# Optimization experiments

Hardware: AMD Instinct MI355X
Metric: run time of the kernel (lower is better)

Reference implementation:

```python
import jax, jax.numpy as jnp
import numpy as np

BSZ, NLVL, E, H, FFN = 8, 4, 512, 8, 2048
D = E // H
NNZ = 131072
LMAX = NNZ // BSZ  # equal per-batch counts -> static padded length
THETA = 10.0


def _layernorm(x, g, b):
    mu = x.mean(-1, keepdims=True)
    var = ((x - mu) ** 2).mean(-1, keepdims=True)
    return (x - mu) / jnp.sqrt(var + 1e-5) * g + b


def _rope(x, pos, freqs):
    # x: [N, E], pos: [N] float, freqs: [H, D/2] -> rotate interleaved pairs per head
    N = x.shape[0]
    nh, half = freqs.shape
    xr = x.reshape(N, nh, half, 2)
    ang = pos[:, None, None] * freqs[None]            # [N, H, D/2]
    c, s = jnp.cos(ang), jnp.sin(ang)
    x1, x2 = xr[..., 0], xr[..., 1]
    out = jnp.stack([x1 * c - x2 * s, x1 * s + x2 * c], axis=-1)
    return out.reshape(N, -1)


def setup_inputs() -> dict:
    key = jax.random.key(0)
    ks = jax.random.split(key, 8)
    bg = jax.random.normal(ks[0], (BSZ, NLVL, E), jnp.float32)
    feature_values = jax.random.normal(ks[1], (NNZ, E), jnp.float32)
    # coalesced sparse COO -> batch indices sorted; equal counts per batch for static shapes
    feature_batch_idx = (jnp.arange(NNZ, dtype=jnp.int32) // LMAX)
    feature_level_idx = jax.random.randint(ks[2], (NNZ,), 0, NLVL, dtype=jnp.int32)
    s = 1.0 / np.sqrt(E)
    Wq = jax.random.normal(ks[3], (E, E), jnp.float32) * s
    Wkv = jax.random.normal(ks[4], (E, 2 * E), jnp.float32) * s
    Wo = jax.random.normal(ks[5], (E, E), jnp.float32) * s
    freqs = THETA ** (-jnp.arange(D // 2, dtype=jnp.float32) * 2.0 / D)
    rope_freqs = jnp.tile(freqs[None, :], (H, 1))  # share_heads=False: per-head table
    ln_attn_g, ln_attn_b = jnp.ones(E, jnp.float32), jnp.zeros(E, jnp.float32)
    ln_ffn_g, ln_ffn_b = jnp.ones(E, jnp.float32), jnp.zeros(E, jnp.float32)
    W1 = jax.random.normal(ks[6], (E, FFN), jnp.float32) * s
    b1 = jnp.zeros(FFN, jnp.float32)
    W2 = jax.random.normal(ks[7], (FFN, E), jnp.float32) * (1.0 / np.sqrt(FFN))
    b2 = jnp.zeros(E, jnp.float32)
    return {
        'bg': bg, 'feature_values': feature_values,
        'feature_batch_idx': feature_batch_idx, 'feature_level_idx': feature_level_idx,
        'Wq': Wq, 'Wkv': Wkv, 'Wo': Wo, 'rope_freqs': rope_freqs,
        'ln_attn_g': ln_attn_g, 'ln_attn_b': ln_attn_b,
        'ln_ffn_g': ln_ffn_g, 'ln_ffn_b': ln_ffn_b,
        'W1': W1, 'b1': b1, 'W2': W2, 'b2': b2,
        'max_len': LMAX,
    }


def reference(bg, feature_values, feature_batch_idx, feature_level_idx,
              Wq, Wkv, Wo, rope_freqs, ln_attn_g, ln_attn_b,
              ln_ffn_g, ln_ffn_b, W1, b1, W2, b2, max_len):
    bsz, nlvl, e = bg.shape
    nh = rope_freqs.shape[0]
    d = e // nh
    nnz = feature_values.shape[0]

    # --- attention block (pre-norm) ---
    residual = bg
    x = _layernorm(bg, ln_attn_g, ln_attn_b)
    q = (x @ Wq).reshape(bsz * nlvl, e)
    kv = feature_values @ Wkv
    k, v = kv[:, :e], kv[:, e:]

    # RoPE on level indices (replicates original's repeat_interleave ordering: level = i // bsz)
    q_lvl = (jnp.arange(bsz * nlvl) // bsz).astype(jnp.float32)
    q = _rope(q, q_lvl, rope_freqs)
    k = _rope(k, feature_level_idx.astype(jnp.float32), rope_freqs)

    # concatenated (ragged) -> padded per batch
    counts = jax.ops.segment_sum(jnp.ones(nnz, jnp.int32), feature_batch_idx, num_segments=bsz)
    offsets = jnp.concatenate([jnp.zeros(1, jnp.int32), jnp.cumsum(counts)[:-1].astype(jnp.int32)])
    pos = jnp.arange(nnz, dtype=jnp.int32) - offsets[feature_batch_idx]
    k_pad = jnp.zeros((bsz, max_len, e), k.dtype).at[feature_batch_idx, pos].set(k)
    v_pad = jnp.zeros((bsz, max_len, e), v.dtype).at[feature_batch_idx, pos].set(v)
    pad_mask = jnp.arange(max_len)[None, :] >= counts[:, None]  # True at padding

    # SDPA
    qh = q.reshape(bsz, nlvl, nh, d).transpose(0, 2, 1, 3)
    kh = k_pad.reshape(bsz, max_len, nh, d).transpose(0, 2, 1, 3)
    vh = v_pad.reshape(bsz, max_len, nh, d).transpose(0, 2, 1, 3)
    scores = jnp.einsum('bhqd,bhkd->bhqk', qh, kh) / jnp.sqrt(jnp.asarray(d, qh.dtype))
    scores = jnp.where(pad_mask[:, None, None, :], -jnp.inf, scores)
    attn = jax.nn.softmax(scores, axis=-1)
    o = jnp.einsum('bhqk,bhkd->bhqd', attn, vh).transpose(0, 2, 1, 3).reshape(bsz, nlvl, e)
    o = o @ Wo + residual

    # --- FFN block (pre-norm) ---
    y = _layernorm(o, ln_ffn_g, ln_ffn_b)
    y = jax.nn.relu(y @ W1 + b1) @ W2 + b2
    return o + y
```

## Files before the change

### kernel.cpp

```cpp
#include <hip/hip_runtime.h>
#include <hip/hip_bf16.h>
#include <math.h>

#define BSZ 8
#define NLVL 4
#define E 512
#define H 8
#define D 64
#define FFN 2048
#define NNZ 131072
#define NQ 32
#define P32 32

typedef __attribute__((ext_vector_type(8))) short bf16x8;
typedef __attribute__((ext_vector_type(4))) float f32x4;

#define WS_QROT   16
#define WS_WSUM   (WS_QROT + NQ*E)
#define WS_OATT   (WS_WSUM + BSZ*P32*E)
#define WS_O2     (WS_OATT + NQ*E)
#define WS_Y      (WS_O2 + NQ*E)
#define WS_HID    (WS_Y + NQ*E)
#define WS_PART   (WS_HID + NQ*FFN)
#define WS_PLANE  (WS_PART + 32*BSZ*P32*E)
#define WS_WALL   (WS_PLANE + P32*NNZ)
#define WS_PBF    (WS_WALL + BSZ*128*512/2)

__device__ inline short f2bf(float x) {
    __hip_bfloat16 h = __float2bfloat16(x);
    union { __hip_bfloat16 v; short s; } u; u.v = h; return u.s;
}

__device__ inline bf16x8 cvt8(const float* p) {
    float4 x = *(const float4*)p;
    float4 y = *(const float4*)(p + 4);
    union { bf16x8 v; __hip_bfloat162 h[4]; } u;
    u.h[0] = __float22bfloat162_rn(float2{x.x, x.y});
    u.h[1] = __float22bfloat162_rn(float2{x.z, x.w});
    u.h[2] = __float22bfloat162_rn(float2{y.x, y.y});
    u.h[3] = __float22bfloat162_rn(float2{y.z, y.w});
    return u.v;
}

__global__ void k_zero(int* wsi) {
    if (blockIdx.x == 0 && threadIdx.x < 8) wsi[threadIdx.x] = 0;
}

__global__ void k_hist(const int* __restrict__ fb, int* wsi) {
    __shared__ int h[8];
    int t = threadIdx.x;
    if (t < 8) h[t] = 0;
    __syncthreads();
    for (int j = blockIdx.x * 256 + t; j < NNZ; j += gridDim.x * 256)
        atomicAdd(&h[fb[j]], 1);
    __syncthreads();
    if (t < 8) atomicAdd(&wsi[t], h[t]);
}

__global__ void k_off(int* wsi) {
    if (threadIdx.x == 0) {
        int run = 0;
        for (int b = 0; b < 8; b++) { wsi[8 + b] = run; run += wsi[b]; }
    }
}

__global__ void k_qrot(const float* __restrict__ bg, const float* __restrict__ Wq,
                       const float* __restrict__ rf, const float* __restrict__ g,
                       const float* __restrict__ bb, float* __restrict__ ws) {
    __shared__ float xr[E];
    __shared__ float qrow[E];
    __shared__ float red[8];
    int r = blockIdx.x, t = threadIdx.x;
    float v0 = bg[r * E + t], v1 = bg[r * E + t + 256];
    float s = v0 + v1;
    for (int o = 32; o > 0; o >>= 1) s += __shfl_down(s, o, 64);
    if ((t & 63) == 0) red[t >> 6] = s;
    __syncthreads();
    if (t == 0) red[0] = (red[0] + red[1] + red[2] + red[3]) * (1.0f / E);
    __syncthreads();
    float mu = red[0];
    __syncthreads();
    float d0 = v0 - mu, d1 = v1 - mu;
    s = d0 * d0 + d1 * d1;
    for (int o = 32; o > 0; o >>= 1) s += __shfl_down(s, o, 64);
    if ((t & 63) == 0) red[t >> 6] = s;
    __syncthreads();
    if (t == 0) red[0] = rsqrtf((red[0] + red[1] + red[2] + red[3]) * (1.0f / E) + 1e-5f);
    __syncthreads();
    float rstd = red[0];
    xr[t] = d0 * rstd * g[t] + bb[t];
    xr[t + 256] = d1 * rstd * g[t + 256] + bb[t + 256];
    __syncthreads();
    for (int half = 0; half < 2; half++) {
        int c = t + half * 256;
        float acc = 0.f;
        for (int e = 0; e < E; e++) acc += xr[e] * Wq[e * E + c];
        qrow[c] = acc;
    }
    __syncthreads();
    int c0 = 2 * t, c1 = c0 + 1;
    int h = c0 >> 6, ii = (c0 & 63) >> 1;
    float freq = rf[h * 32 + ii];
    float pos = (float)(r >> 3);
    float a = pos * freq, ca = cosf(a), sa = sinf(a);
    float x1 = qrow[c0], x2 = qrow[c1];
    float* qr = ws + WS_QROT + r * E;
    qr[c0] = x1 * ca - x2 * sa;
    qr[c1] = x1 * sa + x2 * ca;
}

__global__ void k_wtil(const float* __restrict__ Wkv, const float* __restrict__ rf,
                       const float* __restrict__ ws, short* __restrict__ wall) {
    __shared__ float u[D];
    int blk = blockIdx.x;
    int h = blk & 7, lvl = (blk >> 3) & 3, r = blk >> 5;
    int b = r >> 2, l = r & 3;
    int t = threadIdx.x;
    const float* qr = ws + WS_QROT + r * E + h * D;
    if (t < 32) {
        float freq = rf[h * 32 + t];
        float a = (float)lvl * freq;
        float ca = cosf(a), sa = sinf(a);
        float x1 = qr[2 * t], x2 = qr[2 * t + 1];
        u[2 * t] = x1 * ca + x2 * sa;
        u[2 * t + 1] = -x1 * sa + x2 * ca;
    }
    __syncthreads();
    int n = lvl * 32 + l * 8 + h;
    short* wrow_out = wall + ((size_t)(b * 128 + n)) * E;
    for (int rep = 0; rep < 8; rep++) {
        int e = t + rep * 64;
        const float* wrow = Wkv + (size_t)e * (2 * E) + h * D;
        float acc = 0.f;
#pragma unroll
        for (int c = 0; c < D; c++) acc += wrow[c] * u[c];
        wrow_out[e] = f2bf(acc * 0.125f);
    }
}

__global__ __launch_bounds__(256) void k_scores(
    const float* __restrict__ fv, const int* __restrict__ fb, const int* __restrict__ fl,
    const short* __restrict__ wall, float* __restrict__ pplane) {
    int t = threadIdx.x;
    int wave = t >> 6, lane = t & 63, col = lane & 15, quad = lane >> 4;
    int jbase = blockIdx.x * 128;
    int j0 = jbase + wave * 32;
    int b = fb[jbase];
    const short* wb = wall + (size_t)b * 128 * E + (size_t)col * E + quad * 8;
    const float* a0 = fv + (size_t)(j0 + col) * E + quad * 8;
    const float* a1 = a0 + (size_t)16 * E;
    f32x4 acc[2][8];
#pragma unroll
    for (int mt = 0; mt < 2; mt++)
#pragma unroll
        for (int nt = 0; nt < 8; nt++) acc[mt][nt] = f32x4{0.f, 0.f, 0.f, 0.f};
    for (int ks = 0; ks < 16; ks++) {
        int e0 = ks * 32;
        bf16x8 bfr[8];
#pragma unroll
        for (int nt = 0; nt < 8; nt++)
            bfr[nt] = *(const bf16x8*)(wb + (size_t)nt * 16 * E + e0);
        bf16x8 af0 = cvt8(a0 + e0);
        bf16x8 af1 = cvt8(a1 + e0);
#pragma unroll
        for (int nt = 0; nt < 8; nt++) {
            acc[0][nt] = __builtin_amdgcn_mfma_f32_16x16x32_bf16(af0, bfr[nt], acc[0][nt], 0, 0, 0);
            acc[1][nt] = __builtin_amdgcn_mfma_f32_16x16x32_bf16(af1, bfr[nt], acc[1][nt], 0, 0, 0);
        }
    }
#pragma unroll
    for (int mt = 0; mt < 2; mt++) {
        int kb = j0 + mt * 16 + quad * 4;
#pragma unroll
        for (int r = 0; r < 4; r++) {
            int key = kb + r;
            int lv = fl[key];
#pragma unroll
            for (int nt = 0; nt < 8; nt++) {
                if ((nt >> 1) == lv) {
                    int p = ((nt & 1) << 4) + col;
                    pplane[(size_t)p * NNZ + key] = acc[mt][nt][r];
                }
            }
        }
    }
}

__global__ void k_softmax(const int* __restrict__ wsi, const int* __restrict__ maxlen,
                          float* __restrict__ pplane, short* __restrict__ pbf) {
    __shared__ float red[8];
    int b = blockIdx.x >> 5, p = blockIdx.x & 31;
    int t = threadIdx.x;
    int cnt = wsi[b], ml = maxlen[0];
    int n = cnt < ml ? cnt : ml;
    int off = wsi[8 + b];
    float* base = pplane + (size_t)p * NNZ + off;
    short* basebf = pbf + (size_t)p * NNZ + off;
    float m = -1e30f;
    for (int j = t; j < n; j += 256) m = fmaxf(m, base[j]);
    for (int o = 32; o > 0; o >>= 1) m = fmaxf(m, __shfl_down(m, o, 64));
    if ((t & 63) == 0) red[t >> 6] = m;
    __syncthreads();
    if (t == 0) red[0] = fmaxf(fmaxf(red[0], red[1]), fmaxf(red[2], red[3]));
    __syncthreads();
    m = red[0];
    __syncthreads();
    float s = 0.f;
    for (int j = t; j < n; j += 256) s += expf(base[j] - m);
    for (int o = 32; o > 0; o >>= 1) s += __shfl_down(s, o, 64);
    if ((t & 63) == 0) red[t >> 6] = s;
    __syncthreads();
    if (t == 0) red[0] = red[0] + red[1] + red[2] + red[3];
    __syncthreads();
    float inv = 1.0f / red[0];
    for (int j = t; j < n; j += 256) {
        float w = expf(base[j] - m) * inv;
        base[j] = w;
        basebf[j] = f2bf(w);
    }
}

#define KP 40
__global__ __launch_bounds__(256) void k_pv(
    const float* __restrict__ fv, const short* __restrict__ pbf,
    const int* __restrict__ wsi, const int* __restrict__ maxlen,
    float* __restrict__ part) {
    __shared__ short Bt[256 * KP];
    int t = threadIdx.x;
    int b = blockIdx.x, kc = blockIdx.y, eh = blockIdx.z;
    int cnt = wsi[b], ml = maxlen[0];
    int lim = cnt < ml ? cnt : ml;
    int off = wsi[8 + b];
    int base = kc * 512;
    int wave = t >> 6, lane = t & 63, col = lane & 15, quad = lane >> 4;
    f32x4 acc[2][4];
#pragma unroll
    for (int mt = 0; mt < 2; mt++)
#pragma unroll
        for (int nt = 0; nt < 4; nt++) acc[mt][nt] = f32x4{0.f, 0.f, 0.f, 0.f};
    int nsteps = 0;
    if (base < lim) {
        int r = lim - base;
        nsteps = (r + 31) >> 5;
        if (nsteps > 16) nsteps = 16;
    }
    int sj = (t & 15) * 2;
    int se = (t >> 4) * 16;
    const short* ap0 = pbf + (size_t)col * NNZ + off + base + quad * 8;
    const short* ap1 = ap0 + (size_t)16 * NNZ;
    for (int ks = 0; ks < nsteps; ks++) {
        int kbeg = base + ks * 32;
        __syncthreads();
        {
            int j0g = off + kbeg + sj;
            int j1g = j0g + 1;
            if (j0g > NNZ - 1) j0g = NNZ - 1;
            if (j1g > NNZ - 1) j1g = NNZ - 1;
            const float* r0 = fv + (size_t)j0g * E + eh * 256 + se;
            const float* r1 = fv + (size_t)j1g * E + eh * 256 + se;
#pragma unroll
            for (int i = 0; i < 4; i++) {
                float4 x0 = *(const float4*)(r0 + i * 4);
                float4 x1 = *(const float4*)(r1 + i * 4);
                const float* f0 = (const float*)&x0;
                const float* f1 = (const float*)&x1;
#pragma unroll
                for (int q = 0; q < 4; q++) {
                    *(__hip_bfloat162*)&Bt[(se + i * 4 + q) * KP + sj] =
                        __float22bfloat162_rn(float2{f0[q], f1[q]});
                }
            }
        }
        __syncthreads();
        int rem = lim - kbeg;
        bf16x8 af0 = *(const bf16x8*)(ap0 + ks * 32);
        bf16x8 af1 = *(const bf16x8*)(ap1 + ks * 32);
        if (rem < 32) {
#pragma unroll
            for (int jj = 0; jj < 8; jj++)
                if (quad * 8 + jj >= rem) { af0[jj] = 0; af1[jj] = 0; }
        }
        const short* bb = &Bt[(wave * 64 + col) * KP + quad * 8];
#pragma unroll
        for (int nt = 0; nt < 4; nt++) {
            bf16x8 bfr = *(const bf16x8*)(bb + nt * 16 * KP);
            acc[0][nt] = __builtin_amdgcn_mfma_f32_16x16x32_bf16(af0, bfr, acc[0][nt], 0, 0, 0);
            acc[1][nt] = __builtin_amdgcn_mfma_f32_16x16x32_bf16(af1, bfr, acc[1][nt], 0, 0, 0);
        }
    }
    float* dst = part + ((size_t)(kc * BSZ + b) * P32) * E + eh * 256;
#pragma unroll
    for (int mt = 0; mt < 2; mt++)
#pragma unroll
        for (int nt = 0; nt < 4; nt++)
#pragma unroll
            for (int r = 0; r < 4; r++) {
                int p = mt * 16 + quad * 4 + r;
                int e = wave * 64 + nt * 16 + col;
                dst[(size_t)p * E + e] = acc[mt][nt][r];
            }
}

__global__ void k_pvred(const float* __restrict__ part, float* __restrict__ wsum) {
    int bp = blockIdx.x;
    int t = threadIdx.x;
    int b = bp >> 5, p = bp & 31;
    for (int half = 0; half < 2; half++) {
        int e = t + half * 256;
        float s = 0.f;
        for (int kc = 0; kc < 32; kc++)
            s += part[((size_t)(kc * BSZ + b) * P32 + p) * E + e];
        wsum[(size_t)bp * E + e] = s;
    }
}

__global__ void k_oproj(const float* __restrict__ wsum, const float* __restrict__ Wkv,
                        float* __restrict__ oatt) {
    __shared__ float Aw[NQ][E];
    int h = blockIdx.x >> 2, ct = blockIdx.x & 3;
    int t = threadIdx.x;
    {
        int rr = t >> 3, x = (t & 7) * 64;
        int row = (rr >> 2) * P32 + (rr & 3) * 8 + h;
#pragma unroll
        for (int q4 = 0; q4 < 16; q4++)
            *(float4*)&Aw[rr][x + q4 * 4] = *(const float4*)&wsum[(size_t)row * E + x + q4 * 4];
    }
    __syncthreads();
#pragma unroll
    for (int rep = 0; rep < 2; rep++) {
        int idx = rep * 256 + t;
        int rr = idx >> 4, cl = idx & 15;
        int c = h * D + ct * 16 + cl;
        float acc = 0.f;
        for (int e = 0; e < E; e++) acc += Aw[rr][e] * Wkv[(size_t)e * (2 * E) + E + c];
        oatt[rr * E + c] = acc;
    }
}

__global__ void k_wo(const float* __restrict__ oatt, const float* __restrict__ Wo,
                     const float* __restrict__ bg, float* __restrict__ o2) {
    __shared__ float Aw[NQ * E];
    int t = threadIdx.x;
#pragma unroll
    for (int q = 0; q < 16; q++) {
        int i = (q * 256 + t) * 4;
        *(float4*)&Aw[i] = *(const float4*)&oatt[i];
    }
    __syncthreads();
    int ct = blockIdx.x;
#pragma unroll
    for (int rep = 0; rep < 4; rep++) {
        int idx = rep * 256 + t;
        int rr = idx >> 5, cl = idx & 31;
        int c = ct * 32 + cl;
        float acc = bg[rr * E + c];
        for (int e = 0; e < E; e++) acc += Aw[rr * E + e] * Wo[(size_t)e * E + c];
        o2[rr * E + c] = acc;
    }
}

__global__ void k_ln2(const float* __restrict__ o2, const float* __restrict__ g,
                      const float* __restrict__ bb, float* __restrict__ y) {
    __shared__ float red[8];
    int r = blockIdx.x, t = threadIdx.x;
    float v0 = o2[r * E + t], v1 = o2[r * E + t + 256];
    float s = v0 + v1;
    for (int o = 32; o > 0; o >>= 1) s += __shfl_down(s, o, 64);
    if ((t & 63) == 0) red[t >> 6] = s;
    __syncthreads();
    if (t == 0) red[0] = (red[0] + red[1] + red[2] + red[3]) * (1.0f / E);
    __syncthreads();
    float mu = red[0];
    __syncthreads();
    float d0 = v0 - mu, d1 = v1 - mu;
    s = d0 * d0 + d1 * d1;
    for (int o = 32; o > 0; o >>= 1) s += __shfl_down(s, o, 64);
    if ((t & 63) == 0) red[t >> 6] = s;
    __syncthreads();
    if (t == 0) red[0] = rsqrtf((red[0] + red[1] + red[2] + red[3]) * (1.0f / E) + 1e-5f);
    __syncthreads();
    float rstd = red[0];
    y[r * E + t] = d0 * rstd * g[t] + bb[t];
    y[r * E + t + 256] = d1 * rstd * g[t + 256] + bb[t + 256];
}

__global__ void k_ffn1(const float* __restrict__ y, const float* __restrict__ W1,
                       const float* __restrict__ b1, float* __restrict__ hid) {
    __shared__ float Aw[NQ * E];
    int t = threadIdx.x;
#pragma unroll
    for (int q = 0; q < 16; q++) {
        int i = (q * 256 + t) * 4;
        *(float4*)&Aw[i] = *(const float4*)&y[i];
    }
    __syncthreads();
    int ft = blockIdx.x;
#pragma unroll
    for (int rep = 0; rep < 4; rep++) {
        int idx = rep * 256 + t;
        int rr = idx >> 5, fl = idx & 31;
        int f = ft * 32 + fl;
        float acc = b1[f];
        for (int e = 0; e < E; e++) acc += Aw[rr * E + e] * W1[(size_t)e * FFN + f];
        hid[rr * FFN + f] = fmaxf(acc, 0.f);
    }
}

__global__ void k_ffn2(const float* __restrict__ hid, const float* __restrict__ W2,
                       const float* __restrict__ b2, const float* __restrict__ o2,
                       float* __restrict__ out) {
    int ct = blockIdx.x;
    int t = threadIdx.x;
#pragma unroll
    for (int rep = 0; rep < 2; rep++) {
        int idx = rep * 256 + t;
        int rr = idx >> 4, cl = idx & 15;
        int c = ct * 16 + cl;
        float acc = b2[c] + o2[rr * E + c];
        for (int f = 0; f < FFN; f++) acc += hid[rr * FFN + f] * W2[(size_t)f * E + c];
        out[rr * E + c] = acc;
    }
}

extern "C" void kernel_launch(void* const* d_in, const int* in_sizes, int n_in,
                              void* d_out, int out_size, void* d_ws, size_t ws_size,
                              hipStream_t stream) {
    const float* bg  = (const float*)d_in[0];
    const float* fv  = (const float*)d_in[1];
    const int*   fb  = (const int*)d_in[2];
    const int*   fl  = (const int*)d_in[3];
    const float* Wq  = (const float*)d_in[4];
    const float* Wkv = (const float*)d_in[5];
    const float* Wo  = (const float*)d_in[6];
    const float* rf  = (const float*)d_in[7];
    const float* lag = (const float*)d_in[8];
    const float* lab = (const float*)d_in[9];
    const float* lfg = (const float*)d_in[10];
    const float* lfb = (const float*)d_in[11];
    const float* W1  = (const float*)d_in[12];
    const float* b1  = (const float*)d_in[13];
    const float* W2  = (const float*)d_in[14];
    const float* b2  = (const float*)d_in[15];
    const int* maxlen = (const int*)d_in[16];
    float* ws = (float*)d_ws;
    int* wsi = (int*)d_ws;
    short* wall = (short*)(ws + WS_WALL);
    short* pbf  = (short*)(ws + WS_PBF);
    float* out = (float*)d_out;

    hipLaunchKernelGGL(k_zero, dim3(1), dim3(64), 0, stream, wsi);
    hipLaunchKernelGGL(k_hist, dim3(128), dim3(256), 0, stream, fb, wsi);
    hipLaunchKernelGGL(k_off, dim3(1), dim3(64), 0, stream, wsi);
    hipLaunchKernelGGL(k_qrot, dim3(NQ), dim3(256), 0, stream, bg, Wq, rf, lag, lab, ws);
    hipLaunchKernelGGL(k_wtil, dim3(NQ * NLVL * H), dim3(64), 0, stream, Wkv, rf, ws, wall);
    hipLaunchKernelGGL(k_scores, dim3(NNZ / 128), dim3(256), 0, stream,
                       fv, fb, fl, wall, ws + WS_PLANE);
    hipLaunchKernelGGL(k_softmax, dim3(BSZ * P32), dim3(256), 0, stream,
                       wsi, maxlen, ws + WS_PLANE, pbf);
    hipLaunchKernelGGL(k_pv, dim3(BSZ, 32, 2), dim3(256), 0, stream,
                       fv, pbf, wsi, maxlen, ws + WS_PART);
    hipLaunchKernelGGL(k_pvred, dim3(BSZ * P32), dim3(256), 0, stream,
                       ws + WS_PART, ws + WS_WSUM);
    hipLaunchKernelGGL(k_oproj, dim3(H * 4), dim3(256), 0, stream,
                       ws + WS_WSUM, Wkv, ws + WS_OATT);
    hipLaunchKernelGGL(k_wo, dim3(16), dim3(256), 0, stream,
                       ws + WS_OATT, Wo, bg, ws + WS_O2);
    hipLaunchKernelGGL(k_ln2, dim3(NQ), dim3(256), 0, stream,
                       ws + WS_O2, lfg, lfb, ws + WS_Y);
    hipLaunchKernelGGL(k_ffn1, dim3(FFN / 32), dim3(256), 0, stream,
                       ws + WS_Y, W1, b1, ws + WS_HID);
    hipLaunchKernelGGL(k_ffn2, dim3(E / 16), dim3(256), 0, stream,
                       ws + WS_HID, W2, b2, ws + WS_O2, out);
}
```

Before: 879.0 us.

## Fuse scores, softmax and PV into a flash-style split-K attention kernel

Replaces the separate score GEMM, global softmax and PV kernels with one flash-attention kernel. Each block loads a 256-key chunk of feature values once, converts it to bf16 in shared memory in both row and transposed layouts, and computes scores and PV with an online softmax. Partial outputs and their max/sum statistics are then combined by a merge kernel. This avoids writing and re-reading the fp32 score plane and the bf16 probability plane, and reads the feature values once instead of twice. In exchange it adds more barriers per chunk, heavy shared-memory use, and a larger partial buffer to merge (64 chunks instead of 32).

```diff
diff --git a/kernel.cpp b/kernel.cpp
--- a/kernel.cpp
+++ b/kernel.cpp
@@ -11,6 +11,7 @@
 #define NNZ 131072
 #define NQ 32
 #define P32 32
+#define NEGF -3.0e38f
 
 typedef __attribute__((ext_vector_type(8))) short bf16x8;
 typedef __attribute__((ext_vector_type(4))) float f32x4;
@@ -22,24 +23,12 @@
 #define WS_Y      (WS_O2 + NQ*E)
 #define WS_HID    (WS_Y + NQ*E)
 #define WS_PART   (WS_HID + NQ*FFN)
-#define WS_PLANE  (WS_PART + 32*BSZ*P32*E)
-#define WS_WALL   (WS_PLANE + P32*NNZ)
-#define WS_PBF    (WS_WALL + BSZ*128*512/2)
+#define WS_ML     (WS_PART + 512*P32*E)
+#define WS_WALL   (WS_ML + 512*P32*2)
 
 __device__ inline short f2bf(float x) {
     __hip_bfloat16 h = __float2bfloat16(x);
     union { __hip_bfloat16 v; short s; } u; u.v = h; return u.s;
-}
-
-__device__ inline bf16x8 cvt8(const float* p) {
-    float4 x = *(const float4*)p;
-    float4 y = *(const float4*)(p + 4);
-    union { bf16x8 v; __hip_bfloat162 h[4]; } u;
-    u.h[0] = __float22bfloat162_rn(float2{x.x, x.y});
-    u.h[1] = __float22bfloat162_rn(float2{x.z, x.w});
-    u.h[2] = __float22bfloat162_rn(float2{y.x, y.y});
-    u.h[3] = __float22bfloat162_rn(float2{y.z, y.w});
-    return u.v;
 }
 
 __global__ void k_zero(int* wsi) {
@@ -138,179 +127,227 @@
     }
 }
 
-__global__ __launch_bounds__(256) void k_scores(
-    const float* __restrict__ fv, const int* __restrict__ fb, const int* __restrict__ fl,
-    const short* __restrict__ wall, float* __restrict__ pplane) {
-    int t = threadIdx.x;
-    int wave = t >> 6, lane = t & 63, col = lane & 15, quad = lane >> 4;
-    int jbase = blockIdx.x * 128;
-    int j0 = jbase + wave * 32;
-    int b = fb[jbase];
-    const short* wb = wall + (size_t)b * 128 * E + (size_t)col * E + quad * 8;
-    const float* a0 = fv + (size_t)(j0 + col) * E + quad * 8;
-    const float* a1 = a0 + (size_t)16 * E;
-    f32x4 acc[2][8];
+#define KSTR 520
+#define TSTR 40
+__global__ __launch_bounds__(256, 2) void k_flash(
+    const float* __restrict__ fv, const int* __restrict__ fl,
+    const short* __restrict__ wall, const int* __restrict__ wsi,
+    const int* __restrict__ maxlen, float* __restrict__ part, float* __restrict__ ml) {
+    __shared__ short kbuf[32 * KSTR];
+    __shared__ short fvT[512 * TSTR];
+    __shared__ short pbuf[32 * TSTR];
+    __shared__ float mbuf[4 * 32];
+    __shared__ float lpart[4 * 32];
+    __shared__ float alph[32];
+    __shared__ float mrun[32];
+    __shared__ float lrun[32];
+
+    int t = threadIdx.x;
+    int w = t >> 6, lane = t & 63, col = lane & 15, quad = lane >> 4;
+    int b = blockIdx.x, kc = blockIdx.y;
+    int cnt = wsi[b], mlen = maxlen[0];
+    int lim = cnt < mlen ? cnt : mlen;
+    int off = wsi[8 + b];
+    int kbase = kc * 256;
+    int nv = lim - kbase; if (nv > 256) nv = 256; if (nv < 0) nv = 0;
+
+    if (t < 32) { mrun[t] = NEGF; lrun[t] = 0.f; }
+
+    f32x4 acc_o[2][8];
 #pragma unroll
     for (int mt = 0; mt < 2; mt++)
 #pragma unroll
-        for (int nt = 0; nt < 8; nt++) acc[mt][nt] = f32x4{0.f, 0.f, 0.f, 0.f};
-    for (int ks = 0; ks < 16; ks++) {
-        int e0 = ks * 32;
-        bf16x8 bfr[8];
-#pragma unroll
-        for (int nt = 0; nt < 8; nt++)
-            bfr[nt] = *(const bf16x8*)(wb + (size_t)nt * 16 * E + e0);
-        bf16x8 af0 = cvt8(a0 + e0);
-        bf16x8 af1 = cvt8(a1 + e0);
-#pragma unroll
-        for (int nt = 0; nt < 8; nt++) {
-            acc[0][nt] = __builtin_amdgcn_mfma_f32_16x16x32_bf16(af0, bfr[nt], acc[0][nt], 0, 0, 0);
-            acc[1][nt] = __builtin_amdgcn_mfma_f32_16x16x32_bf16(af1, bfr[nt], acc[1][nt], 0, 0, 0);
-        }
-    }
-#pragma unroll
-    for (int mt = 0; mt < 2; mt++) {
-        int kb = j0 + mt * 16 + quad * 4;
-#pragma unroll
-        for (int r = 0; r < 4; r++) {
-            int key = kb + r;
-            int lv = fl[key];
-#pragma unroll
-            for (int nt = 0; nt < 8; nt++) {
-                if ((nt >> 1) == lv) {
-                    int p = ((nt & 1) << 4) + col;
-                    pplane[(size_t)p * NNZ + key] = acc[mt][nt][r];
-                }
-            }
-        }
-    }
-}
-
-__global__ void k_softmax(const int* __restrict__ wsi, const int* __restrict__ maxlen,
-                          float* __restrict__ pplane, short* __restrict__ pbf) {
-    __shared__ float red[8];
-    int b = blockIdx.x >> 5, p = blockIdx.x & 31;
-    int t = threadIdx.x;
-    int cnt = wsi[b], ml = maxlen[0];
-    int n = cnt < ml ? cnt : ml;
-    int off = wsi[8 + b];
-    float* base = pplane + (size_t)p * NNZ + off;
-    short* basebf = pbf + (size_t)p * NNZ + off;
-    float m = -1e30f;
-    for (int j = t; j < n; j += 256) m = fmaxf(m, base[j]);
-    for (int o = 32; o > 0; o >>= 1) m = fmaxf(m, __shfl_down(m, o, 64));
-    if ((t & 63) == 0) red[t >> 6] = m;
-    __syncthreads();
-    if (t == 0) red[0] = fmaxf(fmaxf(red[0], red[1]), fmaxf(red[2], red[3]));
-    __syncthreads();
-    m = red[0];
-    __syncthreads();
-    float s = 0.f;
-    for (int j = t; j < n; j += 256) s += expf(base[j] - m);
-    for (int o = 32; o > 0; o >>= 1) s += __shfl_down(s, o, 64);
-    if ((t & 63) == 0) red[t >> 6] = s;
-    __syncthreads();
-    if (t == 0) red[0] = red[0] + red[1] + red[2] + red[3];
-    __syncthreads();
-    float inv = 1.0f / red[0];
-    for (int j = t; j < n; j += 256) {
-        float w = expf(base[j] - m) * inv;
-        base[j] = w;
-        basebf[j] = f2bf(w);
-    }
-}
-
-#define KP 40
-__global__ __launch_bounds__(256) void k_pv(
-    const float* __restrict__ fv, const short* __restrict__ pbf,
-    const int* __restrict__ wsi, const int* __restrict__ maxlen,
-    float* __restrict__ part) {
-    __shared__ short Bt[256 * KP];
-    int t = threadIdx.x;
-    int b = blockIdx.x, kc = blockIdx.y, eh = blockIdx.z;
-    int cnt = wsi[b], ml = maxlen[0];
-    int lim = cnt < ml ? cnt : ml;
-    int off = wsi[8 + b];
-    int base = kc * 512;
-    int wave = t >> 6, lane = t & 63, col = lane & 15, quad = lane >> 4;
-    f32x4 acc[2][4];
-#pragma unroll
-    for (int mt = 0; mt < 2; mt++)
-#pragma unroll
-        for (int nt = 0; nt < 4; nt++) acc[mt][nt] = f32x4{0.f, 0.f, 0.f, 0.f};
-    int nsteps = 0;
-    if (base < lim) {
-        int r = lim - base;
-        nsteps = (r + 31) >> 5;
-        if (nsteps > 16) nsteps = 16;
-    }
+        for (int nt = 0; nt < 8; nt++) acc_o[mt][nt] = f32x4{0.f, 0.f, 0.f, 0.f};
+
+    const short* wallb = wall + (size_t)b * 128 * E;
     int sj = (t & 15) * 2;
-    int se = (t >> 4) * 16;
-    const short* ap0 = pbf + (size_t)col * NNZ + off + base + quad * 8;
-    const short* ap1 = ap0 + (size_t)16 * NNZ;
-    for (int ks = 0; ks < nsteps; ks++) {
-        int kbeg = base + ks * 32;
+    int se = (t >> 4) * 32;
+
+    for (int s = 0; s < 8; s++) {
+        int vs = nv - s * 32;
+        if (vs <= 0) break;
         __syncthreads();
         {
-            int j0g = off + kbeg + sj;
-            int j1g = j0g + 1;
-            if (j0g > NNZ - 1) j0g = NNZ - 1;
-            if (j1g > NNZ - 1) j1g = NNZ - 1;
-            const float* r0 = fv + (size_t)j0g * E + eh * 256 + se;
-            const float* r1 = fv + (size_t)j1g * E + eh * 256 + se;
-#pragma unroll
-            for (int i = 0; i < 4; i++) {
+            int g0 = off + kbase + s * 32 + sj;
+            int g1 = g0 + 1;
+            if (g0 > NNZ - 1) g0 = NNZ - 1;
+            if (g1 > NNZ - 1) g1 = NNZ - 1;
+            const float* r0 = fv + (size_t)g0 * E + se;
+            const float* r1 = fv + (size_t)g1 * E + se;
+#pragma unroll
+            for (int i = 0; i < 8; i++) {
                 float4 x0 = *(const float4*)(r0 + i * 4);
                 float4 x1 = *(const float4*)(r1 + i * 4);
-                const float* f0 = (const float*)&x0;
-                const float* f1 = (const float*)&x1;
-#pragma unroll
-                for (int q = 0; q < 4; q++) {
-                    *(__hip_bfloat162*)&Bt[(se + i * 4 + q) * KP + sj] =
-                        __float22bfloat162_rn(float2{f0[q], f1[q]});
-                }
+                int e = se + i * 4;
+                *(__hip_bfloat162*)&kbuf[sj * KSTR + e]       = __float22bfloat162_rn(float2{x0.x, x0.y});
+                *(__hip_bfloat162*)&kbuf[sj * KSTR + e + 2]   = __float22bfloat162_rn(float2{x0.z, x0.w});
+                *(__hip_bfloat162*)&kbuf[(sj+1) * KSTR + e]   = __float22bfloat162_rn(float2{x1.x, x1.y});
+                *(__hip_bfloat162*)&kbuf[(sj+1) * KSTR + e+2] = __float22bfloat162_rn(float2{x1.z, x1.w});
+                *(__hip_bfloat162*)&fvT[(e + 0) * TSTR + sj] = __float22bfloat162_rn(float2{x0.x, x1.x});
+                *(__hip_bfloat162*)&fvT[(e + 1) * TSTR + sj] = __float22bfloat162_rn(float2{x0.y, x1.y});
+                *(__hip_bfloat162*)&fvT[(e + 2) * TSTR + sj] = __float22bfloat162_rn(float2{x0.z, x1.z});
+                *(__hip_bfloat162*)&fvT[(e + 3) * TSTR + sj] = __float22bfloat162_rn(float2{x0.w, x1.w});
             }
         }
         __syncthreads();
-        int rem = lim - kbeg;
-        bf16x8 af0 = *(const bf16x8*)(ap0 + ks * 32);
-        bf16x8 af1 = *(const bf16x8*)(ap1 + ks * 32);
-        if (rem < 32) {
-#pragma unroll
-            for (int jj = 0; jj < 8; jj++)
-                if (quad * 8 + jj >= rem) { af0[jj] = 0; af1[jj] = 0; }
-        }
-        const short* bb = &Bt[(wave * 64 + col) * KP + quad * 8];
-#pragma unroll
-        for (int nt = 0; nt < 4; nt++) {
-            bf16x8 bfr = *(const bf16x8*)(bb + nt * 16 * KP);
-            acc[0][nt] = __builtin_amdgcn_mfma_f32_16x16x32_bf16(af0, bfr, acc[0][nt], 0, 0, 0);
-            acc[1][nt] = __builtin_amdgcn_mfma_f32_16x16x32_bf16(af1, bfr, acc[1][nt], 0, 0, 0);
-        }
-    }
-    float* dst = part + ((size_t)(kc * BSZ + b) * P32) * E + eh * 256;
-#pragma unroll
-    for (int mt = 0; mt < 2; mt++)
-#pragma unroll
-        for (int nt = 0; nt < 4; nt++)
+        f32x4 acc_s[2][2];
+#pragma unroll
+        for (int mt = 0; mt < 2; mt++)
+#pragma unroll
+            for (int kt = 0; kt < 2; kt++) acc_s[mt][kt] = f32x4{0.f, 0.f, 0.f, 0.f};
+        {
+            const short* wr0 = wallb + (size_t)(w * 32 + col) * E + quad * 8;
+            const short* wr1 = wr0 + (size_t)16 * E;
+            const short* kb0 = &kbuf[col * KSTR + quad * 8];
+            const short* kb1 = &kbuf[(16 + col) * KSTR + quad * 8];
+#pragma unroll
+            for (int ks = 0; ks < 16; ks++) {
+                int e0 = ks * 32;
+                bf16x8 A0 = *(const bf16x8*)(wr0 + e0);
+                bf16x8 A1 = *(const bf16x8*)(wr1 + e0);
+                bf16x8 B0 = *(const bf16x8*)(kb0 + e0);
+                bf16x8 B1 = *(const bf16x8*)(kb1 + e0);
+                acc_s[0][0] = __builtin_amdgcn_mfma_f32_16x16x32_bf16(A0, B0, acc_s[0][0], 0, 0, 0);
+                acc_s[0][1] = __builtin_amdgcn_mfma_f32_16x16x32_bf16(A0, B1, acc_s[0][1], 0, 0, 0);
+                acc_s[1][0] = __builtin_amdgcn_mfma_f32_16x16x32_bf16(A1, B0, acc_s[1][0], 0, 0, 0);
+                acc_s[1][1] = __builtin_amdgcn_mfma_f32_16x16x32_bf16(A1, B1, acc_s[1][1], 0, 0, 0);
+            }
+        }
+        int kg0 = off + kbase + s * 32 + col;
+        int kg1 = kg0 + 16;
+        if (kg0 > NNZ - 1) kg0 = NNZ - 1;
+        if (kg1 > NNZ - 1) kg1 = NNZ - 1;
+        int lv0 = fl[kg0], lv1 = fl[kg1];
+        bool valid0 = (s * 32 + col) < nv;
+        bool valid1 = (s * 32 + 16 + col) < nv;
+        bool sel0 = valid0 && (lv0 == w);
+        bool sel1 = valid1 && (lv1 == w);
+#pragma unroll
+        for (int mt = 0; mt < 2; mt++) {
+#pragma unroll
+            for (int r = 0; r < 4; r++) {
+                float v0 = sel0 ? acc_s[mt][0][r] : NEGF;
+                float v1 = sel1 ? acc_s[mt][1][r] : NEGF;
+                float v = fmaxf(v0, v1);
+#pragma unroll
+                for (int msk = 1; msk < 16; msk <<= 1) v = fmaxf(v, __shfl_xor(v, msk, 16));
+                if (col == 0) mbuf[w * 32 + mt * 16 + quad * 4 + r] = v;
+            }
+        }
+        __syncthreads();
+        if (t < 32) {
+            int p = t;
+            float mo = mrun[p];
+            float mn = mo;
+            mn = fmaxf(mn, mbuf[p]);
+            mn = fmaxf(mn, mbuf[32 + p]);
+            mn = fmaxf(mn, mbuf[64 + p]);
+            mn = fmaxf(mn, mbuf[96 + p]);
+            alph[p] = expf(mo - mn);
+            mrun[p] = mn;
+        }
+        __syncthreads();
+        float mr[2][4], ar[2][4];
+#pragma unroll
+        for (int mt = 0; mt < 2; mt++)
 #pragma unroll
             for (int r = 0; r < 4; r++) {
                 int p = mt * 16 + quad * 4 + r;
-                int e = wave * 64 + nt * 16 + col;
-                dst[(size_t)p * E + e] = acc[mt][nt][r];
-            }
-}
-
-__global__ void k_pvred(const float* __restrict__ part, float* __restrict__ wsum) {
-    int bp = blockIdx.x;
-    int t = threadIdx.x;
-    int b = bp >> 5, p = bp & 31;
+                mr[mt][r] = mrun[p];
+                ar[mt][r] = alph[p];
+            }
+#pragma unroll
+        for (int mt = 0; mt < 2; mt++) {
+#pragma unroll
+            for (int r = 0; r < 4; r++) {
+                int p = mt * 16 + quad * 4 + r;
+                float ls = 0.f;
+                {
+                    if (sel0) {
+                        float pv = expf(acc_s[mt][0][r] - mr[mt][r]);
+                        pbuf[p * TSTR + col] = f2bf(pv);
+                        ls += pv;
+                    } else if (w == 0 && !valid0) {
+                        pbuf[p * TSTR + col] = 0;
+                    }
+                    if (sel1) {
+                        float pv = expf(acc_s[mt][1][r] - mr[mt][r]);
+                        pbuf[p * TSTR + 16 + col] = f2bf(pv);
+                        ls += pv;
+                    } else if (w == 0 && !valid1) {
+                        pbuf[p * TSTR + 16 + col] = 0;
+                    }
+                }
+#pragma unroll
+                for (int msk = 1; msk < 16; msk <<= 1) ls += __shfl_xor(ls, msk, 16);
+                if (col == 0) lpart[w * 32 + p] = ls;
+            }
+        }
+#pragma unroll
+        for (int mt = 0; mt < 2; mt++)
+#pragma unroll
+            for (int nt = 0; nt < 8; nt++)
+#pragma unroll
+                for (int r = 0; r < 4; r++) acc_o[mt][nt][r] *= ar[mt][r];
+        __syncthreads();
+        {
+            bf16x8 Ap0 = *(const bf16x8*)&pbuf[col * TSTR + quad * 8];
+            bf16x8 Ap1 = *(const bf16x8*)&pbuf[(16 + col) * TSTR + quad * 8];
+            const short* bt = &fvT[(size_t)(w * 128 + col) * TSTR + quad * 8];
+#pragma unroll
+            for (int nt = 0; nt < 8; nt++) {
+                bf16x8 Bf = *(const bf16x8*)(bt + (size_t)nt * 16 * TSTR);
+                acc_o[0][nt] = __builtin_amdgcn_mfma_f32_16x16x32_bf16(Ap0, Bf, acc_o[0][nt], 0, 0, 0);
+                acc_o[1][nt] = __builtin_amdgcn_mfma_f32_16x16x32_bf16(Ap1, Bf, acc_o[1][nt], 0, 0, 0);
+            }
+        }
+        if (t < 32) {
+            int p = t;
+            lrun[p] = lrun[p] * alph[p] + (lpart[p] + lpart[32 + p] + lpart[64 + p] + lpart[96 + p]);
+        }
+    }
+    size_t pbase = ((size_t)(b * 64 + kc) * P32) * E;
+#pragma unroll
+    for (int mt = 0; mt < 2; mt++)
+#pragma unroll
+        for (int r = 0; r < 4; r++) {
+            int p = mt * 16 + quad * 4 + r;
+#pragma unroll
+            for (int nt = 0; nt < 8; nt++) {
+                int e = w * 128 + nt * 16 + col;
+                part[pbase + (size_t)p * E + e] = acc_o[mt][nt][r];
+            }
+        }
+    if (t < 32) {
+        size_t idx = (size_t)(b * 64 + kc) * P32 + t;
+        ml[idx * 2] = mrun[t];
+        ml[idx * 2 + 1] = lrun[t];
+    }
+}
+
+__global__ void k_merge(const float* __restrict__ part, const float* __restrict__ ml,
+                        float* __restrict__ wsum) {
+    __shared__ float wexp[64];
+    int b = blockIdx.x >> 5, p = blockIdx.x & 31;
+    int t = threadIdx.x;
+    float M = NEGF;
+    for (int kc = 0; kc < 64; kc++)
+        M = fmaxf(M, ml[((size_t)(b * 64 + kc) * P32 + p) * 2]);
+    float denom = 0.f;
+    for (int kc = 0; kc < 64; kc++) {
+        size_t idx = ((size_t)(b * 64 + kc) * P32 + p) * 2;
+        denom += ml[idx + 1] * expf(ml[idx] - M);
+    }
+    if (t < 64)
+        wexp[t] = expf(ml[((size_t)(b * 64 + t) * P32 + p) * 2] - M);
+    __syncthreads();
+    float inv = 1.0f / denom;
     for (int half = 0; half < 2; half++) {
         int e = t + half * 256;
-        float s = 0.f;
-        for (int kc = 0; kc < 32; kc++)
-            s += part[((size_t)(kc * BSZ + b) * P32 + p) * E + e];
-        wsum[(size_t)bp * E + e] = s;
+        float acc = 0.f;
+        for (int kc = 0; kc < 64; kc++)
+            acc += part[((size_t)(b * 64 + kc) * P32 + p) * E + e] * wexp[kc];
+        wsum[((size_t)(b * P32 + p)) * E + e] = acc * inv;
     }
 }
 
@@ -446,7 +483,6 @@
     float* ws = (float*)d_ws;
     int* wsi = (int*)d_ws;
     short* wall = (short*)(ws + WS_WALL);
-    short* pbf  = (short*)(ws + WS_PBF);
     float* out = (float*)d_out;
 
     hipLaunchKernelGGL(k_zero, dim3(1), dim3(64), 0, stream, wsi);
@@ -454,14 +490,10 @@
     hipLaunchKernelGGL(k_off, dim3(1), dim3(64), 0, stream, wsi);
     hipLaunchKernelGGL(k_qrot, dim3(NQ), dim3(256), 0, stream, bg, Wq, rf, lag, lab, ws);
     hipLaunchKernelGGL(k_wtil, dim3(NQ * NLVL * H), dim3(64), 0, stream, Wkv, rf, ws, wall);
-    hipLaunchKernelGGL(k_scores, dim3(NNZ / 128), dim3(256), 0, stream,
-                       fv, fb, fl, wall, ws + WS_PLANE);
-    hipLaunchKernelGGL(k_softmax, dim3(BSZ * P32), dim3(256), 0, stream,
-                       wsi, maxlen, ws + WS_PLANE, pbf);
-    hipLaunchKernelGGL(k_pv, dim3(BSZ, 32, 2), dim3(256), 0, stream,
-                       fv, pbf, wsi, maxlen, ws + WS_PART);
-    hipLaunchKernelGGL(k_pvred, dim3(BSZ * P32), dim3(256), 0, stream,
-                       ws + WS_PART, ws + WS_WSUM);
+    hipLaunchKernelGGL(k_flash, dim3(BSZ, 64), dim3(256), 0, stream,
+                       fv, fl, wall, wsi, maxlen, ws + WS_PART, ws + WS_ML);
+    hipLaunchKernelGGL(k_merge, dim3(BSZ * P32), dim3(256), 0, stream,
+                       ws + WS_PART, ws + WS_ML, ws + WS_WSUM);
     hipLaunchKernelGGL(k_oproj, dim3(H * 4), dim3(256), 0, stream,
                        ws + WS_WSUM, Wkv, ws + WS_OATT);
     hipLaunchKernelGGL(k_wo, dim3(16), dim3(256), 0, stream,
```

Result: no change. 864.2 us (-1.7%).
